# Kernel optimization log

Hardware: AMD Instinct MI355X
Metric: run time of the kernel (lower is better)

## Reference

```python
import jax, jax.numpy as jnp
import numpy as np
from jax import lax
from itertools import product

KS = 3          # kernel_size
PAD = 1         # padding
N = KS ** 3     # 27 sample points per voxel


def _conv3d_3x3(x, w, b):
    # x: [b,c,D,H,W], w: [O,c,3,3,3]
    out = lax.conv_general_dilated(x, w, (1, 1, 1), [(PAD, PAD)] * 3,
                                   dimension_numbers=('NCDHW', 'OIDHW', 'NCDHW'))
    return out + b[None, :, None, None, None]


def setup_inputs() -> dict:
    key = jax.random.key(0)
    k1, k2, k3, k4 = jax.random.split(key, 4)
    B, C, D, OUTC = 2, 32, 24, 64
    x = jax.random.normal(k1, (B, C, D, D, D), jnp.float32)
    p_w = jax.random.normal(k2, (3 * N, C, KS, KS, KS), jnp.float32) * 0.02
    p_b = jax.random.normal(k3, (3 * N,), jnp.float32) * 0.02
    conv_w = jax.random.normal(k4, (OUTC, C * N), jnp.float32) / np.sqrt(C * N)
    return {"x": x, "p_w": p_w, "p_b": p_b, "conv_w": conv_w}


def reference(x, p_w, p_b, conv_w):
    b, c, h, w, d = x.shape
    # offset prediction: [b, 3N, h, w, d]
    offset = _conv3d_3x3(x, p_w, p_b)

    # p_n: kernel-relative offsets, p_0: base grid (shifted by +1 for padding)
    r = np.arange(-(KS - 1) // 2, (KS - 1) // 2 + 1)
    gx, gy, gz = np.meshgrid(r, r, r, indexing='ij')
    p_n = jnp.asarray(np.concatenate([gx.ravel(), gy.ravel(), gz.ravel()])
                      .reshape(1, 3 * N, 1, 1, 1), jnp.float32)
    ox, oy, oz = np.meshgrid(np.arange(1, h + 1), np.arange(1, w + 1),
                             np.arange(1, d + 1), indexing='ij')
    def rep(a):
        return np.broadcast_to(a.reshape(1, 1, h, w, d), (1, N, h, w, d))
    p_0 = jnp.asarray(np.concatenate([rep(ox), rep(oy), rep(oz)], axis=1), jnp.float32)

    p = p_0 + p_n + offset                      # [b, 3N, h, w, d]
    p = jnp.transpose(p, (0, 2, 3, 4, 1))        # [b, h, w, d, 3N]

    xp = jnp.pad(x, ((0, 0), (0, 0), (PAD, PAD), (PAD, PAD), (PAD, PAD)))
    sizes = (xp.shape[2], xp.shape[3], xp.shape[4])
    ps = [p[..., :N], p[..., N:2 * N], p[..., 2 * N:]]

    qs, ql, pm = [], [], []
    for ax in range(3):
        s = sizes[ax]
        f = jnp.floor(ps[ax])
        qs.append(jnp.clip(f, 0, s - 1).astype(jnp.int32))
        ql.append(jnp.clip(f + 1, 0, s - 1).astype(jnp.int32))
        # out-of-range mask: snap p to its floor (matches torch detach + floor_p)
        m = lax.stop_gradient(((ps[ax] < PAD) | (ps[ax] > s - 1 - PAD)).astype(ps[ax].dtype))
        pa = ps[ax] * (1 - m) + f * m
        pm.append(jnp.clip(pa, 0, s - 1))

    def gather(xb, qi, qj, qk):
        return xb[:, qi, qj, qk]  # [c, h, w, d, N]

    acc = jnp.zeros((b, c, h, w, d, N), x.dtype)
    for cx, cy, cz in product((0, 1), repeat=3):   # 8 trilinear corners
        bits = (cx, cy, cz)
        q = [qs[a] if bits[a] == 0 else ql[a] for a in range(3)]
        g = jnp.ones_like(pm[0])
        for a in range(3):
            diff = q[a].astype(pm[a].dtype) - pm[a]
            g = g * ((1 + diff) if bits[a] == 0 else (1 - diff))
        xq = jax.vmap(gather)(xp, q[0], q[1], q[2])  # [b, c, h, w, d, N]
        acc = acc + g[:, None] * xq

    # [b,c,h,w,d,N] -> [b, c*N, h, w, d] (c-major, N-minor, as in torch view)
    x_off = jnp.transpose(acc, (0, 1, 5, 2, 3, 4)).reshape(b, c * N, h, w, d)
    out = jnp.einsum('oi,bidhw->bodhw', conv_w, x_off)
    p_out = jnp.concatenate(pm, axis=-1)
    return out, p_out
```

## Files before the change

### kernel.cpp

```cpp
#include <hip/hip_runtime.h>

#define CC 32
#define DIM 24
#define SP (DIM*DIM*DIM)
#define NPTS 27
#define M3 81
#define OUTC 64
#define BATCH 2
#define CN (CC*NPTS)

#define VBB 12
#define NV (NPTS*VBB)
#define CPAD 896
#define MP 84
#define XR 26
#define HALOF (288*XR)
#define CHUNKF 256

typedef __attribute__((ext_vector_type(8))) short short8;
typedef __attribute__((ext_vector_type(4))) float f32x4;

__device__ __forceinline__ unsigned short f2bf(float f) {
    unsigned u = __builtin_bit_cast(unsigned, f);
    return (unsigned short)((u + 0x7FFFu + ((u >> 16) & 1u)) >> 16);
}

__device__ __forceinline__ void gload16(const float* g, float* l) {
    __builtin_amdgcn_global_load_lds(
        (const __attribute__((address_space(1))) void*)g,
        (__attribute__((address_space(3))) void*)l, 16, 0, 0);
}

__global__ __launch_bounds__(256)
void prep_w_kernel(const float* __restrict__ p_w,
                   const float* __restrict__ conv_w,
                   float* __restrict__ p_wTP,
                   unsigned short* __restrict__ conv_wbf) {
    int id = blockIdx.x * 256 + threadIdx.x;
    if (id < CN * MP) {
        int k = id / MP, m = id % MP;
        p_wTP[id] = (m < M3) ? p_w[(size_t)m * CN + k] : 0.f;
    }
    if (id < CN * OUTC) {
        int o = id / CN, kp = id % CN;
        int n = kp >> 5, c = kp & 31;
        conv_wbf[id] = f2bf(conv_w[(size_t)o * CN + c * NPTS + n]);
    }
}

__global__ __launch_bounds__(256)
void transpose_x_kernel(const float* __restrict__ x,
                        unsigned short* __restrict__ x_t) {
    __shared__ float tile[CC][65];
    int b = blockIdx.x / 216;
    int sp0 = (blockIdx.x % 216) * 64;
    const float* xb = x + (size_t)b * CC * SP;
    for (int it = threadIdx.x; it < CC * 64; it += 256) {
        int c = it >> 6, s = it & 63;
        tile[c][s] = xb[(size_t)c * SP + sp0 + s];
    }
    __syncthreads();
    unsigned short* xtb = x_t + (size_t)b * SP * CC;
    for (int it = threadIdx.x; it < CC * 64; it += 256) {
        int s = it >> 5, c = it & 31;
        xtb[(size_t)(sp0 + s) * CC + c] = f2bf(tile[c][s]);
    }
}

__global__ __launch_bounds__(256, 4)
void offset_gemm_kernel(const float* __restrict__ x,
                        const float* __restrict__ p_wTP,
                        const float* __restrict__ p_b,
                        float* __restrict__ offset) {
    __shared__ __align__(16) float lds[HALOF + 4 * 2 * CHUNKF];

    int bid = blockIdx.x;
    int j = bid % 24;
    int i = (bid / 24) % 24;
    int b = bid / 576;
    int sp0 = i * 576 + j * 24;
    int t = threadIdx.x;

    for (int it = t; it < 288 * 26; it += 256) {
        int row = it / 26, u = it % 26;
        int c = row / 9, dij = row % 9;
        int di = dij / 3, dj = dij % 3;
        int ii = i + di - 1, jj = j + dj - 1, kk = u - 1;
        bool v = ((unsigned)ii < (unsigned)DIM) && ((unsigned)jj < (unsigned)DIM) &&
                 ((unsigned)kk < (unsigned)DIM);
        lds[it] =
            v ? x[((size_t)(b * CC + c) * SP) + ii * 576 + jj * 24 + kk] : 0.f;
    }
    __syncthreads();

    int w = t >> 6, l = t & 63;
    int mt = l / 3, vt = l % 3;
    bool act = (l < 63);
    if (mt > 20) mt = 20;

    float acc[4][8];
    #pragma unroll
    for (int a = 0; a < 4; ++a)
        #pragma unroll
        for (int e = 0; e < 8; ++e) acc[a][e] = 0.f;

    const float* gw = p_wTP + (size_t)(w * 216) * MP;
    const float* xbase = lds + (w * 72) * XR + vt * 8;
    float* cbase = lds + HALOF + w * 2 * CHUNKF;

    #define FMA_BODY(WB, CDIJ)                                              \
        do {                                                                \
            const float* xr = xbase + (CDIJ) * XR;                          \
            float2 x0 = *(const float2*)(xr);                               \
            float2 x1 = *(const float2*)(xr + 2);                           \
            float2 x2 = *(const float2*)(xr + 4);                           \
            float2 x3 = *(const float2*)(xr + 6);                           \
            float2 x4 = *(const float2*)(xr + 8);                           \
            float xv[10] = { x0.x, x0.y, x1.x, x1.y, x2.x, x2.y,            \
                             x3.x, x3.y, x4.x, x4.y };                      \
            _Pragma("unroll")                                               \
            for (int dk = 0; dk < 3; ++dk) {                                \
                float4 wv = *(const float4*)((WB) + dk * MP);               \
                _Pragma("unroll")                                           \
                for (int e = 0; e < 8; ++e) {                               \
                    float xvv = xv[dk + e];                                 \
                    acc[0][e] += wv.x * xvv;                                \
                    acc[1][e] += wv.y * xvv;                                \
                    acc[2][e] += wv.z * xvv;                                \
                    acc[3][e] += wv.w * xvv;                                \
                }                                                           \
            }                                                               \
        } while (0)

    gload16(gw + l * 4, cbase);

    int cur = 0;
    for (int cdij = 0; cdij < 72; ++cdij) {
        gload16(gw + (size_t)(cdij + 1) * 252 + l * 4,
                cbase + (cur ^ 1) * CHUNKF);
        asm volatile("s_waitcnt vmcnt(1)" ::: "memory");
        __builtin_amdgcn_sched_barrier(0);
        FMA_BODY(cbase + cur * CHUNKF + mt * 4, cdij);
        cur ^= 1;
    }
    #undef FMA_BODY
    asm volatile("s_waitcnt vmcnt(0)" ::: "memory");
    __builtin_amdgcn_sched_barrier(0);
    __syncthreads();

    float* part = lds;
    if (act && w < 2) {
        #pragma unroll
        for (int a = 0; a < 4; ++a) {
            #pragma unroll
            for (int e2 = 0; e2 < 2; ++e2) {
                float4 pv = make_float4(acc[a][e2 * 4], acc[a][e2 * 4 + 1],
                                        acc[a][e2 * 4 + 2], acc[a][e2 * 4 + 3]);
                *(float4*)&part[((w * MP) + mt * 4 + a) * 24 + vt * 8 + e2 * 4] = pv;
            }
        }
    }
    __syncthreads();
    if (act && w >= 2) {
        #pragma unroll
        for (int a = 0; a < 4; ++a) {
            #pragma unroll
            for (int e2 = 0; e2 < 2; ++e2) {
                float* dst = &part[(((w - 2) * MP) + mt * 4 + a) * 24 + vt * 8 + e2 * 4];
                float4 pv = *(const float4*)dst;
                pv.x += acc[a][e2 * 4];     pv.y += acc[a][e2 * 4 + 1];
                pv.z += acc[a][e2 * 4 + 2]; pv.w += acc[a][e2 * 4 + 3];
                *(float4*)dst = pv;
            }
        }
    }
    __syncthreads();

    for (int it = t; it < M3 * 6; it += 256) {
        int m = it / 6, vq = it % 6;
        float4 p0 = *(const float4*)&part[(m) * 24 + vq * 4];
        float4 p1 = *(const float4*)&part[(MP + m) * 24 + vq * 4];
        float bias = p_b[m];
        float4 s = make_float4(p0.x + p1.x + bias, p0.y + p1.y + bias,
                               p0.z + p1.z + bias, p0.w + p1.w + bias);
        *(float4*)&offset[((size_t)(b * M3 + m)) * SP + sp0 + vq * 4] = s;
    }
}

__global__ __launch_bounds__(256, 4)
void sample_gemm_kernel(const unsigned short* __restrict__ x_t,
                        const float* __restrict__ offset,
                        const unsigned short* __restrict__ conv_wbf,
                        float* __restrict__ out,
                        float* __restrict__ p_out) {
    __shared__ __align__(16) unsigned char region[VBB * CPAD * 2 + 8 * NV * 4];
    unsigned short* col = (unsigned short*)region;
    unsigned* s_corner = (unsigned*)(region + VBB * CPAD * 2);

    int bid = blockIdx.x;
    int r = bid & 1;
    int j = (bid >> 1) % 24;
    int i = ((bid >> 1) / 24) % 24;
    int b = bid / 1152;
    int k0 = r * VBB;
    int sp0 = i * 576 + j * 24 + k0;
    int t = threadIdx.x;

    const unsigned short* xtb = x_t + (size_t)b * SP * CC;

    for (int it = t; it < NV; it += 256) {
        int v = it % VBB, n = it / VBB;
        int sp = sp0 + v;
        int k = k0 + v;

        int pnx = n / 9 - 1, pny = (n / 3) % 3 - 1, pnz = n % 3 - 1;
        float p0a[3] = { (float)(i + 1 + pnx),
                         (float)(j + 1 + pny),
                         (float)(k + 1 + pnz) };
        int ql[3], qh[3];
        float wl[3], wh[3];
        #pragma unroll
        for (int ax = 0; ax < 3; ++ax) {
            int m = ax * NPTS + n;
            float p = p0a[ax] + offset[((size_t)(b * M3 + m)) * SP + sp];
            float f = floorf(p);
            int qlo = (int)fminf(fmaxf(f,       0.f), 25.f);
            int qhi = (int)fminf(fmaxf(f + 1.f, 0.f), 25.f);
            bool oob = (p < 1.f) || (p > 24.f);
            float pa = oob ? f : p;
            float pm = fminf(fmaxf(pa, 0.f), 25.f);
            ql[ax] = qlo; qh[ax] = qhi;
            wl[ax] = 1.f + ((float)qlo - pm);
            wh[ax] = 1.f - ((float)qhi - pm);
            p_out[((size_t)(b * SP + sp)) * M3 + m] = pm;
        }

        #pragma unroll
        for (int cr = 0; cr < 8; ++cr) {
            int ii = ((cr & 4) ? qh[0] : ql[0]) - 1;
            int jj = ((cr & 2) ? qh[1] : ql[1]) - 1;
            int kk = ((cr & 1) ? qh[2] : ql[2]) - 1;
            bool valid = ((unsigned)ii < (unsigned)DIM) &&
                         ((unsigned)jj < (unsigned)DIM) &&
                         ((unsigned)kk < (unsigned)DIM);
            float cw = ((cr & 4) ? wh[0] : wl[0]) *
                       ((cr & 2) ? wh[1] : wl[1]) *
                       ((cr & 1) ? wh[2] : wl[2]);
            unsigned idx = (unsigned)(ii * 576 + jj * 24 + kk);
            s_corner[cr * NV + it] =
                valid ? ((idx << 16) | (unsigned)f2bf(cw)) : 0u;
        }
    }
    __syncthreads();

    for (int task = t; task < NV * 4; task += 256) {
        int item = task >> 2, q = task & 3;
        int v = item % VBB, n = item / VBB;

        const unsigned short* xq = xtb + q * 8;
        float acc[8];
        #pragma unroll
        for (int e = 0; e < 8; ++e) acc[e] = 0.f;

        #pragma unroll
        for (int cr = 0; cr < 8; ++cr) {
            unsigned u = s_corner[cr * NV + item];
            float wc = __builtin_bit_cast(float, u << 16);
            const unsigned* s = (const unsigned*)(xq + (size_t)(u >> 16) * CC);
            #pragma unroll
            for (int q2 = 0; q2 < 4; ++q2) {
                unsigned uu = s[q2];
                acc[2 * q2]     += wc * __builtin_bit_cast(float, uu << 16);
                acc[2 * q2 + 1] += wc * __builtin_bit_cast(float, uu & 0xFFFF0000u);
            }
        }

        short8 pk;
        #pragma unroll
        for (int e = 0; e < 8; ++e)
            pk[e] = (short)f2bf(acc[e]);
        int sv = (v & 7) << 3;
        *(short8*)&col[v * CPAD + ((n * 32 + q * 8) ^ sv)] = pk;
    }
    __syncthreads();

    {
        int mt = t >> 6;
        int l = t & 63;
        int lr = l & 15;
        int g = l >> 4;
        int sv = (lr & 7) << 3;

        const short8* ap =
            (const short8*)(conv_wbf + ((size_t)(mt * 16 + lr)) * CN + g * 8);
        const unsigned short* bp = col + lr * CPAD;

        f32x4 acc = {0.f, 0.f, 0.f, 0.f};
        #pragma unroll 3
        for (int kb = 0; kb < CN / 32; ++kb) {
            short8 a = ap[kb * 4];
            short8 bb = *(const short8*)&bp[(kb * 32 + g * 8) ^ sv];
            acc = __builtin_amdgcn_mfma_f32_16x16x32_bf16(a, bb, acc, 0, 0, 0);
        }
        if (lr < VBB) {
            float* op = out + ((size_t)(b * OUTC + mt * 16 + g * 4)) * SP + sp0 + lr;
            #pragma unroll
            for (int rr = 0; rr < 4; ++rr)
                op[(size_t)rr * SP] = acc[rr];
        }
    }
}

extern "C" void kernel_launch(void* const* d_in, const int* in_sizes, int n_in,
                              void* d_out, int out_size, void* d_ws, size_t ws_size,
                              hipStream_t stream) {
    const float* x      = (const float*)d_in[0];
    const float* p_w    = (const float*)d_in[1];
    const float* p_b    = (const float*)d_in[2];
    const float* conv_w = (const float*)d_in[3];

    float* out_all = (float*)d_out;
    float* out_main = out_all;
    float* p_out    = out_all + (size_t)BATCH * OUTC * SP;

    float* offset          = (float*)d_ws;
    float* p_wTP           = offset + (size_t)BATCH * M3 * SP;
    unsigned short* conv_wbf = (unsigned short*)(p_wTP + (size_t)CN * MP);
    unsigned short* x_t    = conv_wbf + (size_t)CN * OUTC;

    {
        int total = CN * MP;
        prep_w_kernel<<<(total + 255) / 256, 256, 0, stream>>>(p_w, conv_w,
                                                               p_wTP, conv_wbf);
    }
    {
        int blocks = BATCH * (SP / 64);
        transpose_x_kernel<<<blocks, 256, 0, stream>>>(x, x_t);
    }
    {
        int blocks = BATCH * 24 * 24;
        offset_gemm_kernel<<<blocks, 256, 0, stream>>>(x, p_wTP, p_b, offset);
    }
    {
        int blocks = BATCH * 24 * 24 * 2;
        sample_gemm_kernel<<<blocks, 256, 0, stream>>>(x_t, offset, conv_wbf,
                                                       out_main, p_out);
    }
}
```

Before: 132.7 us.

## Compute two output rows per block in offset conv, reading weights directly from global

The offset-prediction conv kernel now handles two adjacent j-rows per block, with 512 threads split into 8 waves over channel groups, and loads a shared 4-row halo. Each weight float4 is reused for both rows via doubled accumulators. The LDS double-buffered async weight prefetch is dropped in favour of direct global/cached loads. The aim is to halve weight traffic per output and improve reuse, at the cost of more registers, a four-stage cross-wave reduction with extra barriers, and fewer blocks.

```diff
diff --git a/kernel.cpp b/kernel.cpp
--- a/kernel.cpp
+++ b/kernel.cpp
@@ -13,9 +13,8 @@
 #define NV (NPTS*VBB)
 #define CPAD 896
 #define MP 84
-#define XR 26
-#define HALOF (288*XR)
-#define CHUNKF 256
+#define HROW 26
+#define HALOF (32*3*4*HROW)
 
 typedef __attribute__((ext_vector_type(8))) short short8;
 typedef __attribute__((ext_vector_type(4))) float f32x4;
@@ -23,12 +22,6 @@
 __device__ __forceinline__ unsigned short f2bf(float f) {
     unsigned u = __builtin_bit_cast(unsigned, f);
     return (unsigned short)((u + 0x7FFFu + ((u >> 16) & 1u)) >> 16);
-}
-
-__device__ __forceinline__ void gload16(const float* g, float* l) {
-    __builtin_amdgcn_global_load_lds(
-        (const __attribute__((address_space(1))) void*)g,
-        (__attribute__((address_space(3))) void*)l, 16, 0, 0);
 }
 
 __global__ __launch_bounds__(256)
@@ -67,25 +60,26 @@
     }
 }
 
-__global__ __launch_bounds__(256, 4)
+__global__ __launch_bounds__(512, 4)
 void offset_gemm_kernel(const float* __restrict__ x,
                         const float* __restrict__ p_wTP,
                         const float* __restrict__ p_b,
                         float* __restrict__ offset) {
-    __shared__ __align__(16) float lds[HALOF + 4 * 2 * CHUNKF];
+    __shared__ float lds[HALOF];
 
     int bid = blockIdx.x;
-    int j = bid % 24;
-    int i = (bid / 24) % 24;
-    int b = bid / 576;
-    int sp0 = i * 576 + j * 24;
+    int jp = bid % 12;
+    int i  = (bid / 12) % 24;
+    int b  = bid / 288;
+    int j0 = jp * 2;
+    int sp0 = i * 576 + j0 * 24;
     int t = threadIdx.x;
 
-    for (int it = t; it < 288 * 26; it += 256) {
-        int row = it / 26, u = it % 26;
-        int c = row / 9, dij = row % 9;
-        int di = dij / 3, dj = dij % 3;
-        int ii = i + di - 1, jj = j + dj - 1, kk = u - 1;
+    for (int it = t; it < HALOF; it += 512) {
+        int rh = it / HROW, u = it - rh * HROW;
+        int c = rh / 12, r2 = rh - c * 12;
+        int di = r2 >> 2, jq = r2 & 3;
+        int ii = i + di - 1, jj = j0 - 1 + jq, kk = u - 1;
         bool v = ((unsigned)ii < (unsigned)DIM) && ((unsigned)jj < (unsigned)DIM) &&
                  ((unsigned)kk < (unsigned)DIM);
         lds[it] =
@@ -98,88 +92,104 @@
     bool act = (l < 63);
     if (mt > 20) mt = 20;
 
-    float acc[4][8];
+    float acc[4][8], ac2[4][8];
     #pragma unroll
     for (int a = 0; a < 4; ++a)
         #pragma unroll
-        for (int e = 0; e < 8; ++e) acc[a][e] = 0.f;
-
-    const float* gw = p_wTP + (size_t)(w * 216) * MP;
-    const float* xbase = lds + (w * 72) * XR + vt * 8;
-    float* cbase = lds + HALOF + w * 2 * CHUNKF;
-
-    #define FMA_BODY(WB, CDIJ)                                              \
+        for (int e = 0; e < 8; ++e) { acc[a][e] = 0.f; ac2[a][e] = 0.f; }
+
+    const float* gw = p_wTP + (size_t)(w * 108) * MP + mt * 4;
+
+    for (int cdij = 0; cdij < 36; ++cdij) {
+        int c = 4 * w + cdij / 9;
+        int dij = cdij % 9;
+        int di = dij / 3, dj = dij % 3;
+        const float* xrA = lds + ((c * 3 + di) * 4 + dj) * HROW + vt * 8;
+        const float* xrB = xrA + HROW;
+
+        float2 a0 = *(const float2*)(xrA);
+        float2 a1 = *(const float2*)(xrA + 2);
+        float2 a2 = *(const float2*)(xrA + 4);
+        float2 a3 = *(const float2*)(xrA + 6);
+        float2 a4 = *(const float2*)(xrA + 8);
+        float xvA[10] = { a0.x, a0.y, a1.x, a1.y, a2.x, a2.y,
+                          a3.x, a3.y, a4.x, a4.y };
+        float2 b0 = *(const float2*)(xrB);
+        float2 b1 = *(const float2*)(xrB + 2);
+        float2 b2 = *(const float2*)(xrB + 4);
+        float2 b3 = *(const float2*)(xrB + 6);
+        float2 b4 = *(const float2*)(xrB + 8);
+        float xvB[10] = { b0.x, b0.y, b1.x, b1.y, b2.x, b2.y,
+                          b3.x, b3.y, b4.x, b4.y };
+
+        const float* wr = gw + (size_t)(cdij * 3) * MP;
+        #pragma unroll
+        for (int dk = 0; dk < 3; ++dk) {
+            float4 wv = *(const float4*)(wr + (size_t)dk * MP);
+            #pragma unroll
+            for (int e = 0; e < 8; ++e) {
+                float xa = xvA[dk + e];
+                float xb = xvB[dk + e];
+                acc[0][e] += wv.x * xa;  ac2[0][e] += wv.x * xb;
+                acc[1][e] += wv.y * xa;  ac2[1][e] += wv.y * xb;
+                acc[2][e] += wv.z * xa;  ac2[2][e] += wv.z * xb;
+                acc[3][e] += wv.w * xa;  ac2[3][e] += wv.w * xb;
+            }
+        }
+    }
+    __syncthreads();
+
+    float* part = lds;
+    #define STORE_P(W)                                                      \
         do {                                                                \
-            const float* xr = xbase + (CDIJ) * XR;                          \
-            float2 x0 = *(const float2*)(xr);                               \
-            float2 x1 = *(const float2*)(xr + 2);                           \
-            float2 x2 = *(const float2*)(xr + 4);                           \
-            float2 x3 = *(const float2*)(xr + 6);                           \
-            float2 x4 = *(const float2*)(xr + 8);                           \
-            float xv[10] = { x0.x, x0.y, x1.x, x1.y, x2.x, x2.y,            \
-                             x3.x, x3.y, x4.x, x4.y };                      \
+            float* dst = &part[((W) * MP + mt * 4) * 48 + vt * 8];          \
             _Pragma("unroll")                                               \
-            for (int dk = 0; dk < 3; ++dk) {                                \
-                float4 wv = *(const float4*)((WB) + dk * MP);               \
+            for (int a = 0; a < 4; ++a) {                                   \
                 _Pragma("unroll")                                           \
-                for (int e = 0; e < 8; ++e) {                               \
-                    float xvv = xv[dk + e];                                 \
-                    acc[0][e] += wv.x * xvv;                                \
-                    acc[1][e] += wv.y * xvv;                                \
-                    acc[2][e] += wv.z * xvv;                                \
-                    acc[3][e] += wv.w * xvv;                                \
+                for (int e2 = 0; e2 < 2; ++e2) {                            \
+                    *(float4*)&dst[a * 48 + e2 * 4] =                       \
+                        make_float4(acc[a][e2*4], acc[a][e2*4+1],           \
+                                    acc[a][e2*4+2], acc[a][e2*4+3]);        \
+                    *(float4*)&dst[a * 48 + 24 + e2 * 4] =                  \
+                        make_float4(ac2[a][e2*4], ac2[a][e2*4+1],           \
+                                    ac2[a][e2*4+2], ac2[a][e2*4+3]);        \
                 }                                                           \
             }                                                               \
         } while (0)
-
-    gload16(gw + l * 4, cbase);
-
-    int cur = 0;
-    for (int cdij = 0; cdij < 72; ++cdij) {
-        gload16(gw + (size_t)(cdij + 1) * 252 + l * 4,
-                cbase + (cur ^ 1) * CHUNKF);
-        asm volatile("s_waitcnt vmcnt(1)" ::: "memory");
-        __builtin_amdgcn_sched_barrier(0);
-        FMA_BODY(cbase + cur * CHUNKF + mt * 4, cdij);
-        cur ^= 1;
-    }
-    #undef FMA_BODY
-    asm volatile("s_waitcnt vmcnt(0)" ::: "memory");
-    __builtin_amdgcn_sched_barrier(0);
-    __syncthreads();
-
-    float* part = lds;
-    if (act && w < 2) {
-        #pragma unroll
-        for (int a = 0; a < 4; ++a) {
-            #pragma unroll
-            for (int e2 = 0; e2 < 2; ++e2) {
-                float4 pv = make_float4(acc[a][e2 * 4], acc[a][e2 * 4 + 1],
-                                        acc[a][e2 * 4 + 2], acc[a][e2 * 4 + 3]);
-                *(float4*)&part[((w * MP) + mt * 4 + a) * 24 + vt * 8 + e2 * 4] = pv;
-            }
-        }
-    }
-    __syncthreads();
-    if (act && w >= 2) {
-        #pragma unroll
-        for (int a = 0; a < 4; ++a) {
-            #pragma unroll
-            for (int e2 = 0; e2 < 2; ++e2) {
-                float* dst = &part[(((w - 2) * MP) + mt * 4 + a) * 24 + vt * 8 + e2 * 4];
-                float4 pv = *(const float4*)dst;
-                pv.x += acc[a][e2 * 4];     pv.y += acc[a][e2 * 4 + 1];
-                pv.z += acc[a][e2 * 4 + 2]; pv.w += acc[a][e2 * 4 + 3];
-                *(float4*)dst = pv;
-            }
-        }
-    }
-    __syncthreads();
-
-    for (int it = t; it < M3 * 6; it += 256) {
-        int m = it / 6, vq = it % 6;
-        float4 p0 = *(const float4*)&part[(m) * 24 + vq * 4];
-        float4 p1 = *(const float4*)&part[(MP + m) * 24 + vq * 4];
+    #define ADD_P(W)                                                       \
+        do {                                                                \
+            float* dst = &part[((W) * MP + mt * 4) * 48 + vt * 8];          \
+            _Pragma("unroll")                                               \
+            for (int a = 0; a < 4; ++a) {                                   \
+                _Pragma("unroll")                                           \
+                for (int e2 = 0; e2 < 2; ++e2) {                            \
+                    float4 p = *(const float4*)&dst[a * 48 + e2 * 4];       \
+                    p.x += acc[a][e2*4];   p.y += acc[a][e2*4+1];           \
+                    p.z += acc[a][e2*4+2]; p.w += acc[a][e2*4+3];           \
+                    *(float4*)&dst[a * 48 + e2 * 4] = p;                    \
+                    float4 q = *(const float4*)&dst[a * 48 + 24 + e2 * 4];  \
+                    q.x += ac2[a][e2*4];   q.y += ac2[a][e2*4+1];           \
+                    q.z += ac2[a][e2*4+2]; q.w += ac2[a][e2*4+3];           \
+                    *(float4*)&dst[a * 48 + 24 + e2 * 4] = q;               \
+                }                                                           \
+            }                                                               \
+        } while (0)
+
+    if (act && w < 2) STORE_P(w);
+    __syncthreads();
+    if (act && (w == 2 || w == 3)) ADD_P(w - 2);
+    __syncthreads();
+    if (act && (w == 4 || w == 5)) ADD_P(w - 4);
+    __syncthreads();
+    if (act && (w == 6 || w == 7)) ADD_P(w - 6);
+    __syncthreads();
+    #undef STORE_P
+    #undef ADD_P
+
+    for (int it = t; it < M3 * 12; it += 512) {
+        int m = it / 12, vq = it % 12;
+        float4 p0 = *(const float4*)&part[(m) * 48 + vq * 4];
+        float4 p1 = *(const float4*)&part[(MP + m) * 48 + vq * 4];
         float bias = p_b[m];
         float4 s = make_float4(p0.x + p1.x + bias, p0.y + p1.y + bias,
                                p0.z + p1.z + bias, p0.w + p1.w + bias);
@@ -338,8 +348,8 @@
         transpose_x_kernel<<<blocks, 256, 0, stream>>>(x, x_t);
     }
     {
-        int blocks = BATCH * 24 * 24;
-        offset_gemm_kernel<<<blocks, 256, 0, stream>>>(x, p_wTP, p_b, offset);
+        int blocks = BATCH * 24 * 12;
+        offset_gemm_kernel<<<blocks, 512, 0, stream>>>(x, p_wTP, p_b, offset);
     }
     {
         int blocks = BATCH * 24 * 24 * 2;
```

Result: faster. 123.5 us (-7.0%).
